# Performance work log

Hardware: AMD Instinct MI355X
Metric: run time of the kernel (lower is better)

The kernel has to match this reference:

```python
import jax, jax.numpy as jnp
import numpy as np

B, N, D, NH, NL = 256, 1001, 128, 8, 3  # bsz, nb_nodes+1, dim_emb, nb_heads, n_decode_layers
CLIP = 10.0


def setup_inputs() -> dict:
    key = jax.random.key(0)
    ks = jax.random.split(key, 8)
    h_t = jax.random.normal(ks[0], (B, D), jnp.float32)
    K_att = jax.random.normal(ks[1], (B, N, NL * D), jnp.float32)
    V_att = jax.random.normal(ks[2], (B, N, NL * D), jnp.float32)
    mask = jax.random.bernoulli(ks[3], 0.5, (B, N))  # True = visited (masked out)
    W = jax.random.normal(ks[4], (NL - 1, 8, D, D), jnp.float32) * 0.05
    b = jax.random.normal(ks[5], (NL - 1, 8, D), jnp.float32) * 0.05
    ln_g = jnp.ones((NL - 1, 3, D), jnp.float32)
    ln_b = jnp.zeros((NL - 1, 3, D), jnp.float32)
    Wq_final = jax.random.normal(ks[6], (D, D), jnp.float32) * 0.05
    bq_final = jax.random.normal(ks[7], (D,), jnp.float32) * 0.05
    return {"h_t": h_t, "K_att": K_att, "V_att": V_att, "mask": mask,
            "W": W, "b": b, "ln_g": ln_g, "ln_b": ln_b,
            "Wq_final": Wq_final, "bq_final": bq_final}


def _layernorm(x, g, bb):
    m = x.mean(-1, keepdims=True)
    v = ((x - m) ** 2).mean(-1, keepdims=True)
    return (x - m) / jnp.sqrt(v + 1e-5) * g + bb


def _mha(Q, K, V, nh, mask=None, clip=None):
    # Q: (B,1,Dm), K,V: (B,S,Dm); faithful to myMHA (head split, tanh clip, mask, softmax)
    Bq, S, Dm = K.shape
    dh = Dm // nh
    q = Q.reshape(Bq, 1, nh, dh).transpose(0, 2, 1, 3)   # (B,h,1,dh)
    k = K.reshape(Bq, S, nh, dh).transpose(0, 2, 1, 3)   # (B,h,S,dh)
    v = V.reshape(Bq, S, nh, dh).transpose(0, 2, 1, 3)
    s = jnp.einsum('bhqd,bhsd->bhqs', q, k) / jnp.sqrt(jnp.float32(dh))
    if clip is not None:
        s = clip * jnp.tanh(s)
    if mask is not None:
        s = jnp.where(mask[:, None, None, :], jnp.float32(-1e9), s)
    w = jax.nn.softmax(s, axis=-1)                        # (B,h,1,S)
    out = jnp.einsum('bhqs,bhsd->bhqd', w, v)
    out = out.transpose(0, 2, 1, 3).reshape(Bq, 1, Dm)    # concat heads
    return out, w.mean(axis=1)                            # (B,1,Dm), (B,1,S)


def reference(h_t, K_att, V_att, mask, W, b, ln_g, ln_b, Wq_final, bq_final):
    h = h_t  # (B,D)
    probs = None
    for l in range(NL):
        Kl = K_att[:, :, l * D:(l + 1) * D]
        Vl = V_att[:, :, l * D:(l + 1) * D]
        if l < NL - 1:
            Wl, bl = W[l], b[l]
            hq = h[:, None, :]                                      # (B,1,D)
            # self-attention (first decode step: keys/values are just this token)
            q_sa = hq @ Wl[0] + bl[0]
            k_sa = hq @ Wl[1] + bl[1]
            v_sa = hq @ Wl[2] + bl[2]
            sa, _ = _mha(q_sa, k_sa, v_sa, NH)
            h = _layernorm((hq + sa @ Wl[3] + bl[3])[:, 0, :], ln_g[l, 0], ln_b[l, 0])
            # query attention over graph nodes with visited-mask
            hq = h[:, None, :]
            q_a = hq @ Wl[4] + bl[4]
            at, _ = _mha(q_a, Kl, Vl, NH, mask)
            h = _layernorm((hq + at @ Wl[5] + bl[5])[:, 0, :], ln_g[l, 1], ln_b[l, 1])
            # MLP
            h = _layernorm(h + jax.nn.relu(h @ Wl[6] + bl[6]) @ Wl[7] + bl[7], ln_g[l, 2], ln_b[l, 2])
        else:
            q_f = (h @ Wq_final + bq_final)[:, None, :]
            _, aw = _mha(q_f, Kl, Vl, 1, mask, CLIP)
            probs = aw[:, 0, :]                                     # (B,N)
    return probs
```

## Files before the change

kernel.cpp:

```cpp
#include <hip/hip_runtime.h>
#include <math.h>

#define NB 256
#define NN 1001
#define DD 128
#define SP 1008

__device__ __forceinline__ float wsum(float v) {
  #pragma unroll
  for (int off = 32; off > 0; off >>= 1) v += __shfl_xor(v, off, 64);
  return v;
}
__device__ __forceinline__ float wmax(float v) {
  #pragma unroll
  for (int off = 32; off > 0; off >>= 1) v = fmaxf(v, __shfl_xor(v, off, 64));
  return v;
}

__device__ void matvec(const float* __restrict__ Wm, const float* __restrict__ bias,
                       const float* in_s, const float* res_s, float* out_s,
                       float* part, int t, bool relu) {
  const int j = t & 127;
  const int half = t >> 7;
  const float* __restrict__ col = Wm + (size_t)half * 64 * DD + j;
  const float* in = in_s + half * 64;
  float acc = 0.f;
  #pragma unroll 8
  for (int i = 0; i < 64; ++i) acc = fmaf(in[i], col[(size_t)i * DD], acc);
  part[t] = acc;
  __syncthreads();
  if (t < 128) {
    float v = part[t] + part[t + 128] + bias[t];
    if (res_s) v += res_s[t];
    if (relu) v = fmaxf(v, 0.f);
    out_s[t] = v;
  }
  __syncthreads();
}

__device__ void lnorm(const float* t_s, float* h_s, const float* __restrict__ g,
                      const float* __restrict__ bb, float* red, int t) {
  const int wid = t >> 6, lane = t & 63;
  float x = (t < 128) ? t_s[t] : 0.f;
  float s = wsum(x);
  if (lane == 0) red[wid] = s;
  __syncthreads();
  float mean = (red[0] + red[1] + red[2] + red[3]) * (1.f / 128.f);
  float d = (t < 128) ? (x - mean) : 0.f;
  float s2 = wsum(d * d);
  if (lane == 0) red[4 + wid] = s2;
  __syncthreads();
  float var = (red[4] + red[5] + red[6] + red[7]) * (1.f / 128.f);
  if (t < 128) h_s[t] = d * rsqrtf(var + 1e-5f) * g[t] + bb[t];
  __syncthreads();
}

extern "C" __global__ void __launch_bounds__(256)
attn_model_kernel(const float* __restrict__ h_t, const float* __restrict__ K_att,
                  const float* __restrict__ V_att, const int* __restrict__ mask,
                  const float* __restrict__ W, const float* __restrict__ bW,
                  const float* __restrict__ ln_g, const float* __restrict__ ln_b,
                  const float* __restrict__ Wq, const float* __restrict__ bq,
                  float* __restrict__ out) {
  __shared__ __align__(16) float scores[8 * SP];
  __shared__ float h_s[DD], q_s[DD], tmp_s[DD], t_s[DD];
  __shared__ float part[256];
  __shared__ __align__(16) float vred[8 * DD];
  __shared__ float red[8];
  __shared__ float hsum[8];

  const int t = threadIdx.x;
  const int b = blockIdx.x;
  const int wid = t >> 6, lane = t & 63;

  if (t < 128) h_s[t] = h_t[(size_t)b * DD + t];
  __syncthreads();

  const int* __restrict__ mb = mask + (size_t)b * NN;

  for (int l = 0; l < 2; ++l) {
    const float* Wl = W + (size_t)l * 8 * DD * DD;
    const float* bl = bW + (size_t)l * 8 * DD;

    matvec(Wl + 2 * DD * DD, bl + 2 * DD, h_s, nullptr, tmp_s, part, t, false);
    matvec(Wl + 3 * DD * DD, bl + 3 * DD, tmp_s, h_s, t_s, part, t, false);
    lnorm(t_s, h_s, ln_g + (l * 3 + 0) * DD, ln_b + (l * 3 + 0) * DD, red, t);
    matvec(Wl + 4 * DD * DD, bl + 4 * DD, h_s, nullptr, q_s, part, t, false);

    const float* Kb = K_att + (size_t)b * NN * 384 + l * DD;
    const float* Vb = V_att + (size_t)b * NN * 384 + l * DD;
    {
      const int nl0 = t >> 3, hh = t & 7;
      float qr[16];
      #pragma unroll
      for (int k = 0; k < 16; ++k) qr[k] = q_s[hh * 16 + k];
      for (int base = 0; base < 1024; base += 32) {
        int n = base + nl0;
        if (n < NN) {
          const float4* kr = (const float4*)(Kb + (size_t)n * 384 + hh * 16);
          float4 a0 = kr[0], a1 = kr[1], a2 = kr[2], a3 = kr[3];
          float sacc = a0.x*qr[0] + a0.y*qr[1] + a0.z*qr[2] + a0.w*qr[3]
                     + a1.x*qr[4] + a1.y*qr[5] + a1.z*qr[6] + a1.w*qr[7]
                     + a2.x*qr[8] + a2.y*qr[9] + a2.z*qr[10] + a2.w*qr[11]
                     + a3.x*qr[12] + a3.y*qr[13] + a3.z*qr[14] + a3.w*qr[15];
          float sc = sacc * 0.25f;
          if (mb[n] != 0) sc = -1e9f;
          scores[hh * SP + n] = sc;
        }
      }
      __syncthreads();

      #pragma unroll
      for (int ho = 0; ho < 2; ++ho) {
        int h2 = 2 * wid + ho;
        float m = -1e30f;
        for (int n = lane; n < NN; n += 64) m = fmaxf(m, scores[h2 * SP + n]);
        m = wmax(m);
        float ss = 0.f;
        for (int n = lane; n < NN; n += 64) {
          float e = __expf(scores[h2 * SP + n] - m);
          scores[h2 * SP + n] = e;
          ss += e;
        }
        ss = wsum(ss);
        if (lane == 0) hsum[h2] = 1.f / ss;
      }
      __syncthreads();

      const int g = t >> 5, c4 = t & 31, hv = c4 >> 2;
      float4 acc = make_float4(0.f, 0.f, 0.f, 0.f);
      for (int n = g; n < NN; n += 8) {
        float w = scores[hv * SP + n];
        const float4 vv = *(const float4*)(Vb + (size_t)n * 384 + c4 * 4);
        acc.x = fmaf(w, vv.x, acc.x);
        acc.y = fmaf(w, vv.y, acc.y);
        acc.z = fmaf(w, vv.z, acc.z);
        acc.w = fmaf(w, vv.w, acc.w);
      }
      *(float4*)(vred + g * DD + c4 * 4) = acc;
      __syncthreads();
      if (t < 128) {
        float at = 0.f;
        #pragma unroll
        for (int gg = 0; gg < 8; ++gg) at += vred[gg * DD + t];
        tmp_s[t] = at * hsum[t >> 4];
      }
      __syncthreads();
    }

    matvec(Wl + 5 * DD * DD, bl + 5 * DD, tmp_s, h_s, t_s, part, t, false);
    lnorm(t_s, h_s, ln_g + (l * 3 + 1) * DD, ln_b + (l * 3 + 1) * DD, red, t);
    matvec(Wl + 6 * DD * DD, bl + 6 * DD, h_s, nullptr, tmp_s, part, t, true);
    matvec(Wl + 7 * DD * DD, bl + 7 * DD, tmp_s, h_s, t_s, part, t, false);
    lnorm(t_s, h_s, ln_g + (l * 3 + 2) * DD, ln_b + (l * 3 + 2) * DD, red, t);
  }

  matvec(Wq, bq, h_s, nullptr, q_s, part, t, false);
  {
    const float* Kb = K_att + (size_t)b * NN * 384 + 2 * DD;
    const int nl0 = t >> 3, p8 = t & 7;
    float qr[16];
    #pragma unroll
    for (int k = 0; k < 16; ++k) qr[k] = q_s[p8 * 16 + k];
    float* fs = scores;
    for (int base = 0; base < 1024; base += 32) {
      int n = base + nl0;
      float sacc = 0.f;
      if (n < NN) {
        const float4* kr = (const float4*)(Kb + (size_t)n * 384 + p8 * 16);
        float4 a0 = kr[0], a1 = kr[1], a2 = kr[2], a3 = kr[3];
        sacc = a0.x*qr[0] + a0.y*qr[1] + a0.z*qr[2] + a0.w*qr[3]
             + a1.x*qr[4] + a1.y*qr[5] + a1.z*qr[6] + a1.w*qr[7]
             + a2.x*qr[8] + a2.y*qr[9] + a2.z*qr[10] + a2.w*qr[11]
             + a3.x*qr[12] + a3.y*qr[13] + a3.z*qr[14] + a3.w*qr[15];
      }
      sacc += __shfl_xor(sacc, 1, 64);
      sacc += __shfl_xor(sacc, 2, 64);
      sacc += __shfl_xor(sacc, 4, 64);
      if (n < NN && p8 == 0) {
        float sc = sacc * 0.08838834764831845f;
        sc = 10.f * tanhf(sc);
        if (mb[n] != 0) sc = -1e9f;
        fs[n] = sc;
      }
    }
    __syncthreads();

    float m = -1e30f;
    for (int n = t; n < NN; n += 256) m = fmaxf(m, fs[n]);
    m = wmax(m);
    if (lane == 0) red[wid] = m;
    __syncthreads();
    m = fmaxf(fmaxf(red[0], red[1]), fmaxf(red[2], red[3]));
    float ss = 0.f;
    for (int n = t; n < NN; n += 256) {
      float e = __expf(fs[n] - m);
      fs[n] = e;
      ss += e;
    }
    ss = wsum(ss);
    if (lane == 0) red[4 + wid] = ss;
    __syncthreads();
    float inv = 1.f / (red[4] + red[5] + red[6] + red[7]);
    for (int n = t; n < NN; n += 256) out[(size_t)b * NN + n] = fs[n] * inv;
  }
}

extern "C" void kernel_launch(void* const* d_in, const int* in_sizes, int n_in,
                              void* d_out, int out_size, void* d_ws, size_t ws_size,
                              hipStream_t stream) {
  const float* h_t   = (const float*)d_in[0];
  const float* K_att = (const float*)d_in[1];
  const float* V_att = (const float*)d_in[2];
  const int*   mask  = (const int*)d_in[3];
  const float* W     = (const float*)d_in[4];
  const float* bW    = (const float*)d_in[5];
  const float* ln_g  = (const float*)d_in[6];
  const float* ln_b  = (const float*)d_in[7];
  const float* Wq    = (const float*)d_in[8];
  const float* bq    = (const float*)d_in[9];
  float* out = (float*)d_out;

  hipLaunchKernelGGL(attn_model_kernel, dim3(NB), dim3(256), 0, stream,
                     h_t, K_att, V_att, mask, W, bW, ln_g, ln_b, Wq, bq, out);
}
```

Baseline: 867.8 us.

## Widen blocks to 1024 threads and repartition all phases across 16 waves

Raises the block from 256 to 1024 threads while keeping one block per batch row, and rebalances each stage to match. Matvecs split the input into 8 slices of 16, score loops stride by 128 nodes and are fully unrolled, per-head softmax uses two waves per head, V accumulation uses 32 groups, and the final softmax gives each thread one node. The aim is more memory parallelism per CU, since only 256 blocks run on a large GPU. In exchange there are more barriers, larger shared reduction buffers, and register pressure under the 1024-thread launch bound.

After: 748.9 us. 13.7% less time.

```diff
diff --git a/kernel.cpp b/kernel.cpp
--- a/kernel.cpp
+++ b/kernel.cpp
@@ -5,6 +5,7 @@
 #define NN 1001
 #define DD 128
 #define SP 1008
+#define BT 1024
 
 __device__ __forceinline__ float wsum(float v) {
   #pragma unroll
@@ -21,16 +22,18 @@
                        const float* in_s, const float* res_s, float* out_s,
                        float* part, int t, bool relu) {
   const int j = t & 127;
-  const int half = t >> 7;
-  const float* __restrict__ col = Wm + (size_t)half * 64 * DD + j;
-  const float* in = in_s + half * 64;
+  const int slice = t >> 7;
+  const float* __restrict__ col = Wm + (size_t)slice * 16 * DD + j;
+  const float* in = in_s + slice * 16;
   float acc = 0.f;
-  #pragma unroll 8
-  for (int i = 0; i < 64; ++i) acc = fmaf(in[i], col[(size_t)i * DD], acc);
+  #pragma unroll
+  for (int i = 0; i < 16; ++i) acc = fmaf(in[i], col[(size_t)i * DD], acc);
   part[t] = acc;
   __syncthreads();
   if (t < 128) {
-    float v = part[t] + part[t + 128] + bias[t];
+    float v = bias[t];
+    #pragma unroll
+    for (int g = 0; g < 8; ++g) v += part[t + g * 128];
     if (res_s) v += res_s[t];
     if (relu) v = fmaxf(v, 0.f);
     out_s[t] = v;
@@ -45,17 +48,17 @@
   float s = wsum(x);
   if (lane == 0) red[wid] = s;
   __syncthreads();
-  float mean = (red[0] + red[1] + red[2] + red[3]) * (1.f / 128.f);
+  float mean = (red[0] + red[1]) * (1.f / 128.f);
   float d = (t < 128) ? (x - mean) : 0.f;
   float s2 = wsum(d * d);
-  if (lane == 0) red[4 + wid] = s2;
-  __syncthreads();
-  float var = (red[4] + red[5] + red[6] + red[7]) * (1.f / 128.f);
+  if (lane == 0) red[wid] = s2;
+  __syncthreads();
+  float var = (red[0] + red[1]) * (1.f / 128.f);
   if (t < 128) h_s[t] = d * rsqrtf(var + 1e-5f) * g[t] + bb[t];
   __syncthreads();
 }
 
-extern "C" __global__ void __launch_bounds__(256)
+extern "C" __global__ void __launch_bounds__(BT)
 attn_model_kernel(const float* __restrict__ h_t, const float* __restrict__ K_att,
                   const float* __restrict__ V_att, const int* __restrict__ mask,
                   const float* __restrict__ W, const float* __restrict__ bW,
@@ -63,10 +66,10 @@
                   const float* __restrict__ Wq, const float* __restrict__ bq,
                   float* __restrict__ out) {
   __shared__ __align__(16) float scores[8 * SP];
+  __shared__ __align__(16) float vred[32 * DD];
+  __shared__ float part[BT];
   __shared__ float h_s[DD], q_s[DD], tmp_s[DD], t_s[DD];
-  __shared__ float part[256];
-  __shared__ __align__(16) float vred[8 * DD];
-  __shared__ float red[8];
+  __shared__ float wred[16], wred2[16];
   __shared__ float hsum[8];
 
   const int t = threadIdx.x;
@@ -84,7 +87,7 @@
 
     matvec(Wl + 2 * DD * DD, bl + 2 * DD, h_s, nullptr, tmp_s, part, t, false);
     matvec(Wl + 3 * DD * DD, bl + 3 * DD, tmp_s, h_s, t_s, part, t, false);
-    lnorm(t_s, h_s, ln_g + (l * 3 + 0) * DD, ln_b + (l * 3 + 0) * DD, red, t);
+    lnorm(t_s, h_s, ln_g + (l * 3 + 0) * DD, ln_b + (l * 3 + 0) * DD, wred, t);
     matvec(Wl + 4 * DD * DD, bl + 4 * DD, h_s, nullptr, q_s, part, t, false);
 
     const float* Kb = K_att + (size_t)b * NN * 384 + l * DD;
@@ -94,7 +97,8 @@
       float qr[16];
       #pragma unroll
       for (int k = 0; k < 16; ++k) qr[k] = q_s[hh * 16 + k];
-      for (int base = 0; base < 1024; base += 32) {
+      #pragma unroll
+      for (int base = 0; base < 1024; base += 128) {
         int n = base + nl0;
         if (n < NN) {
           const float4* kr = (const float4*)(Kb + (size_t)n * 384 + hh * 16);
@@ -110,26 +114,31 @@
       }
       __syncthreads();
 
-      #pragma unroll
-      for (int ho = 0; ho < 2; ++ho) {
-        int h2 = 2 * wid + ho;
+      {
+        const int h2 = wid >> 1, half = wid & 1;
         float m = -1e30f;
-        for (int n = lane; n < NN; n += 64) m = fmaxf(m, scores[h2 * SP + n]);
+        for (int n = 64 * half + lane; n < NN; n += 128)
+          m = fmaxf(m, scores[h2 * SP + n]);
         m = wmax(m);
+        if (lane == 0) wred[wid] = m;
+        __syncthreads();
+        float mm = fmaxf(wred[2 * h2], wred[2 * h2 + 1]);
         float ss = 0.f;
-        for (int n = lane; n < NN; n += 64) {
-          float e = __expf(scores[h2 * SP + n] - m);
+        for (int n = 64 * half + lane; n < NN; n += 128) {
+          float e = __expf(scores[h2 * SP + n] - mm);
           scores[h2 * SP + n] = e;
           ss += e;
         }
         ss = wsum(ss);
-        if (lane == 0) hsum[h2] = 1.f / ss;
-      }
-      __syncthreads();
+        if (lane == 0) wred2[wid] = ss;
+        __syncthreads();
+        if (t < 8) hsum[t] = 1.f / (wred2[2 * t] + wred2[2 * t + 1]);
+        __syncthreads();
+      }
 
       const int g = t >> 5, c4 = t & 31, hv = c4 >> 2;
       float4 acc = make_float4(0.f, 0.f, 0.f, 0.f);
-      for (int n = g; n < NN; n += 8) {
+      for (int n = g; n < NN; n += 32) {
         float w = scores[hv * SP + n];
         const float4 vv = *(const float4*)(Vb + (size_t)n * 384 + c4 * 4);
         acc.x = fmaf(w, vv.x, acc.x);
@@ -142,17 +151,17 @@
       if (t < 128) {
         float at = 0.f;
         #pragma unroll
-        for (int gg = 0; gg < 8; ++gg) at += vred[gg * DD + t];
+        for (int gg = 0; gg < 32; ++gg) at += vred[gg * DD + t];
         tmp_s[t] = at * hsum[t >> 4];
       }
       __syncthreads();
     }
 
     matvec(Wl + 5 * DD * DD, bl + 5 * DD, tmp_s, h_s, t_s, part, t, false);
-    lnorm(t_s, h_s, ln_g + (l * 3 + 1) * DD, ln_b + (l * 3 + 1) * DD, red, t);
+    lnorm(t_s, h_s, ln_g + (l * 3 + 1) * DD, ln_b + (l * 3 + 1) * DD, wred, t);
     matvec(Wl + 6 * DD * DD, bl + 6 * DD, h_s, nullptr, tmp_s, part, t, true);
     matvec(Wl + 7 * DD * DD, bl + 7 * DD, tmp_s, h_s, t_s, part, t, false);
-    lnorm(t_s, h_s, ln_g + (l * 3 + 2) * DD, ln_b + (l * 3 + 2) * DD, red, t);
+    lnorm(t_s, h_s, ln_g + (l * 3 + 2) * DD, ln_b + (l * 3 + 2) * DD, wred, t);
   }
 
   matvec(Wq, bq, h_s, nullptr, q_s, part, t, false);
@@ -163,7 +172,8 @@
     #pragma unroll
     for (int k = 0; k < 16; ++k) qr[k] = q_s[p8 * 16 + k];
     float* fs = scores;
-    for (int base = 0; base < 1024; base += 32) {
+    #pragma unroll
+    for (int base = 0; base < 1024; base += 128) {
       int n = base + nl0;
       float sacc = 0.f;
       if (n < NN) {
@@ -186,23 +196,21 @@
     }
     __syncthreads();
 
-    float m = -1e30f;
-    for (int n = t; n < NN; n += 256) m = fmaxf(m, fs[n]);
-    m = wmax(m);
-    if (lane == 0) red[wid] = m;
+    float v = (t < NN) ? fs[t] : -1e30f;
+    float m = wmax(v);
+    if (lane == 0) wred[wid] = m;
     __syncthreads();
-    m = fmaxf(fmaxf(red[0], red[1]), fmaxf(red[2], red[3]));
-    float ss = 0.f;
-    for (int n = t; n < NN; n += 256) {
-      float e = __expf(fs[n] - m);
-      fs[n] = e;
-      ss += e;
-    }
-    ss = wsum(ss);
-    if (lane == 0) red[4 + wid] = ss;
+    float mm = -1e30f;
+    #pragma unroll
+    for (int i = 0; i < 16; ++i) mm = fmaxf(mm, wred[i]);
+    float e = (t < NN) ? __expf(v - mm) : 0.f;
+    float ss = wsum(e);
+    if (lane == 0) wred2[wid] = ss;
     __syncthreads();
-    float inv = 1.f / (red[4] + red[5] + red[6] + red[7]);
-    for (int n = t; n < NN; n += 256) out[(size_t)b * NN + n] = fs[n] * inv;
+    float tot = 0.f;
+    #pragma unroll
+    for (int i = 0; i < 16; ++i) tot += wred2[i];
+    if (t < NN) out[(size_t)b * NN + t] = e * (1.f / tot);
   }
 }
 
@@ -221,6 +229,6 @@
   const float* bq    = (const float*)d_in[9];
   float* out = (float*)d_out;
 
-  hipLaunchKernelGGL(attn_model_kernel, dim3(NB), dim3(256), 0, stream,
+  hipLaunchKernelGGL(attn_model_kernel, dim3(NB), dim3(BT), 0, stream,
                      h_t, K_att, V_att, mask, W, bW, ln_g, ln_b, Wq, bq, out);
 }
```
